# Kernel optimization log

Hardware: AMD Instinct MI355X
Metric: run time of the kernel (lower is better)

## Reference

```python
import jax, jax.numpy as jnp
import numpy as np

IN_F = 256
OUT_F = 256
ALPHA = 0.2  # LeakyReLU negative slope


def _xavier(key, shape, gain=1.414):
    fan_in, fan_out = shape[0], shape[1]
    limit = gain * np.sqrt(6.0 / (fan_in + fan_out))
    return jax.random.uniform(key, shape, jnp.float32, -limit, limit)


def setup_inputs() -> dict:
    key = jax.random.key(0)
    k1, k2, k3, k4, k5, k6 = jax.random.split(key, 6)
    B, N = 8, 2048
    h = jax.random.normal(k1, (B, N, IN_F), jnp.float32)
    adj = jax.random.randint(k2, (B, N, N), 0, 2, jnp.int32)
    lrgt1 = jax.random.normal(k3, (B, N, OUT_F), jnp.float32)
    W1 = _xavier(k4, (IN_F, IN_F))
    W2 = _xavier(k5, (OUT_F, OUT_F))
    a = _xavier(k6, (2 * IN_F, 1))
    return {"h": h, "adj": adj, "lrgt1": lrgt1, "W1": W1, "W2": W2, "a": a}


def reference(h, adj, lrgt1, W1, W2, a):
    # Wh: [B,N,in], wlrgt: [B,N,out]
    Wh = jnp.matmul(h, W1)
    wlrgt = jnp.matmul(lrgt1, W2)
    # additive attention scores: e[b,i,j] = leaky_relu(Wh_i @ a1 + Wh_j @ a2)
    a1 = a[:IN_F, 0]   # [in]
    a2 = a[IN_F:, 0]   # [in]
    Wh1 = jnp.einsum('bnc,c->bn', Wh, a1)  # [B,N]
    Wh2 = jnp.einsum('bnc,c->bn', Wh, a2)  # [B,N]
    e = jax.nn.leaky_relu(Wh1[:, :, None] + Wh2[:, None, :], ALPHA)  # [B,N,N]
    neg = jnp.float32(-9e15)
    masked = jnp.where(adj > 0, e, neg)
    attention = jax.nn.softmax(masked, axis=2)
    # dropout p=0.0 / eval mode -> identity
    h_prime = jnp.matmul(attention, Wh)      # [B,N,in]
    gt_prime = jnp.matmul(attention, wlrgt)  # [B,N,out]
    return (jax.nn.elu(h_prime), jax.nn.elu(gt_prime))
```

## Files before the change

kernel.cpp:

```cpp
#include <hip/hip_runtime.h>
#include <hip/hip_bf16.h>

#define IN_F 256
#define NN   2048
#define BB   8

typedef unsigned short u16;
typedef unsigned long long u64;
typedef __attribute__((ext_vector_type(8))) short short8x;
typedef __attribute__((ext_vector_type(4))) float float4x;

__device__ __forceinline__ u16 f2b(float f) {
    union { float f; unsigned int u; } x; x.f = f;
    unsigned int r = x.u + 0x7FFFu + ((x.u >> 16) & 1u);
    return (u16)(r >> 16);
}

__global__ __launch_bounds__(256) void adjpack(const int* __restrict__ adj,
                                               u64* __restrict__ mask)
{
    const int wid  = (blockIdx.x * 256 + threadIdx.x) >> 6;
    const int lane = threadIdx.x & 63;
#pragma unroll 4
    for (int it = 0; it < 64; ++it) {
        const long s = (long)it * 8192 + wid;
        const int v = __builtin_nontemporal_load(adj + s * 64 + lane);
        const u64 m = __ballot(v > 0);
        if (lane == 0) mask[s] = m;
    }
}

__device__ __forceinline__ void transp_body4(const float* __restrict__ src,
                                             u16* __restrict__ dst,
                                             int R, int C, int tid,
                                             float (*tile)[33])
{
    const int per = (R / 32) * (C / 32);
    const int b  = tid / per;
    const int tt = tid % per;
    const int jt = tt / (C / 32);
    const int ct = tt % (C / 32);
    src += (long)b * R * C;
    dst += (long)b * R * C;

    const int t = threadIdx.x;
    const int lr = t >> 3, lc = (t & 7) * 4;
    float4 v = *(const float4*)(src + (long)(jt * 32 + lr) * C + ct * 32 + lc);
    tile[lr][lc + 0] = v.x;
    tile[lr][lc + 1] = v.y;
    tile[lr][lc + 2] = v.z;
    tile[lr][lc + 3] = v.w;
    __syncthreads();
    const int c = t >> 3, r4 = (t & 7) * 4;
    ushort4 o;
    o.x = f2b(tile[r4 + 0][c]);
    o.y = f2b(tile[r4 + 1][c]);
    o.z = f2b(tile[r4 + 2][c]);
    o.w = f2b(tile[r4 + 3][c]);
    *(ushort4*)(dst + (long)(ct * 32 + c) * R + jt * 32 + r4) = o;
}

__global__ __launch_bounds__(256) void prep(const float* __restrict__ h,
                                            const float* __restrict__ g,
                                            const float* __restrict__ W1,
                                            const float* __restrict__ W2,
                                            const float* __restrict__ a,
                                            u16* __restrict__ HbfT,
                                            u16* __restrict__ GbfT,
                                            u16* __restrict__ W1T,
                                            u16* __restrict__ W2T,
                                            float* __restrict__ v1,
                                            float* __restrict__ v2)
{
    __shared__ float tile[32][33];
    __shared__ float s1[IN_F], s2[IN_F];
    const int bid = blockIdx.x;

    if (bid < 4096) {
        transp_body4(h, HbfT, NN, IN_F, bid, tile);
    } else if (bid < 8192) {
        transp_body4(g, GbfT, NN, IN_F, bid - 4096, tile);
    } else if (bid < 8256) {
        transp_body4(W1, W1T, IN_F, IN_F, bid - 8192, tile);
    } else if (bid < 8320) {
        transp_body4(W2, W2T, IN_F, IN_F, bid - 8256, tile);
    } else {
        const int t = threadIdx.x;
        s1[t] = a[t];
        s2[t] = a[IN_F + t];
        __syncthreads();
        float acc1 = 0.f, acc2 = 0.f;
        for (int c = 0; c < IN_F; ++c) {
            float w = W1[t * IN_F + c];
            acc1 += w * s1[c];
            acc2 += w * s2[c];
        }
        v1[t] = acc1;
        v2[t] = acc2;
    }
}

__global__ __launch_bounds__(256) void rowdots(const float* __restrict__ h,
                                               const float* __restrict__ v1,
                                               const float* __restrict__ v2,
                                               float* __restrict__ Wh1,
                                               float* __restrict__ Wh2)
{
    const int wave = threadIdx.x >> 6;
    const int lane = threadIdx.x & 63;
    const long row = (long)blockIdx.x * 4 + wave;
    const int c0 = lane * 4;

    float4 v  = *(const float4*)(h + row * IN_F + c0);
    float4 a1 = *(const float4*)(v1 + c0);
    float4 a2 = *(const float4*)(v2 + c0);

    float s1 = v.x * a1.x + v.y * a1.y + v.z * a1.z + v.w * a1.w;
    float s2 = v.x * a2.x + v.y * a2.y + v.z * a2.z + v.w * a2.w;
#pragma unroll
    for (int off = 32; off; off >>= 1) {
        s1 += __shfl_xor(s1, off, 64);
        s2 += __shfl_xor(s2, off, 64);
    }
    if (lane == 0) { Wh1[row] = s1; Wh2[row] = s2; }
}

#define KSTEP(ksv, BC, BN_, AC, AN_, do_a, jnxt)                              \
    {                                                                         \
        if (do_a) {                                                           \
            _Pragma("unroll") for (int rt = 0; rt < 4; ++rt)                  \
                AN_[rt] = *(const short8x*)&ab[(((ksv) + 1) * 4 + rt) * 512 + lane * 8]; \
        }                                                                     \
        _Pragma("unroll") for (int ct = 0; ct < 4; ++ct)                      \
            BN_[ct] = *(const short8x*)(Bp + ct * 16 * NN + (jnxt));          \
        _Pragma("unroll") for (int rt = 0; rt < 4; ++rt)                      \
            _Pragma("unroll") for (int ct = 0; ct < 4; ++ct)                  \
                acc[rt][ct] = __builtin_amdgcn_mfma_f32_16x16x32_bf16(AC[rt], BC[ct], acc[rt][ct], 0, 0, 0); \
    }

#define CHUNK9(KCH, MKC, MKN)                                                 \
    {                                                                         \
        const int j0 = (KCH) * 128;                                           \
        const unsigned bits = (MKC) >> ((sg & 1) * 16);                       \
        union { short8x v; u16 e[8]; } pk0, pk1;                              \
        _Pragma("unroll") for (int u = 0; u < 4; ++u) {                       \
            const float4 wv = *(const float4*)&wh2L[j0 + sg * 16 + u * 4];    \
            const float wf[4] = {wv.x, wv.y, wv.z, wv.w};                     \
            _Pragma("unroll") for (int c = 0; c < 4; ++c) {                   \
                float x = wh1rr + wf[c];                                      \
                float ev = fmaxf(x, 0.2f * x);                                \
                float p = __expf(ev - mv);                                    \
                p = ((bits >> (u * 4 + c)) & 1u) ? p : 0.0f;                  \
                lloc += p;                                                    \
                u16 fv = f2b(p);                                              \
                if (u < 2) pk0.e[u * 4 + c] = fv;                             \
                else       pk1.e[(u - 2) * 4 + c] = fv;                       \
            }                                                                 \
        }                                                                     \
        if ((KCH) < 15) MKN = maskR[((KCH) + 1) * 4 + (sg >> 1)];             \
        u16* ab = &Afrag[(KCH) & 1][0];                                       \
        *(short8x*)&ab[wbase0]       = pk0.v;                                 \
        *(short8x*)&ab[wbase0 + 128] = pk1.v;                                 \
        asm volatile("s_waitcnt lgkmcnt(0)\n\ts_barrier" ::: "memory");       \
        _Pragma("unroll") for (int rt = 0; rt < 4; ++rt)                      \
            A0[rt] = *(const short8x*)&ab[rt * 512 + lane * 8];               \
        KSTEP(0, B0, B1, A0, A1, 1, j0 + 1 * 32 + bq8)                        \
        KSTEP(1, B1, B0, A1, A0, 1, j0 + 2 * 32 + bq8)                        \
        KSTEP(2, B0, B1, A0, A1, 1, j0 + 3 * 32 + bq8)                        \
        KSTEP(3, B1, B0, A1, A0, 0, (((KCH) < 15) ? (j0 + 128) : j0) + bq8)   \
    }

__global__ __launch_bounds__(512, 2) void attn_mfma(
    const unsigned* __restrict__ mask,
    const u16* __restrict__ HbfT, const u16* __restrict__ GbfT,
    const float* __restrict__ Wh1, const float* __restrict__ Wh2,
    u16* __restrict__ PH, u16* __restrict__ PG)
{
    const int t = threadIdx.x;
    const int wave = t >> 6, lane = t & 63;
    const int bswz = ((blockIdx.x & 7) << 5) | (blockIdx.x >> 3);
    const int b = bswz >> 5;
    const long gi0 = (long)bswz * 64;

    __shared__ __align__(16) u16 Afrag[2][8192];
    __shared__ float wh2L[2048];
    __shared__ float sred[512];
    __shared__ float ssc[65];

    const int rr = t >> 3, sg = t & 7;
    const float* wh2b = Wh2 + (long)b * NN;
    const float wh1rr = Wh1[gi0 + rr];
    const unsigned* maskR = mask + (gi0 + rr) * 64;

    {
        float4 w = *(const float4*)(wh2b + t * 4);
        *(float4*)&wh2L[t * 4] = w;
        sred[t] = fmaxf(fmaxf(w.x, w.y), fmaxf(w.z, w.w));
    }
    __syncthreads();
    if (t < 64) {
        float v = sred[t * 8];
#pragma unroll
        for (int k = 1; k < 8; ++k) v = fmaxf(v, sred[t * 8 + k]);
#pragma unroll
        for (int off = 32; off; off >>= 1) v = fmaxf(v, __shfl_xor(v, off, 64));
        if (t == 0) ssc[64] = v;
    }
    __syncthreads();
    const float mm = wh1rr + ssc[64];
    const float mv = (mm >= 0.f) ? mm : 0.2f * mm;

    const int wbase0 = ((sg >> 1) * 4 + (rr >> 4)) * 512
                     + ((rr & 15) + 16 * (2 * (sg & 1))) * 8;

    float4x acc[4][4];
#pragma unroll
    for (int rt = 0; rt < 4; ++rt)
#pragma unroll
        for (int ct = 0; ct < 4; ++ct) acc[rt][ct] = (float4x)0.0f;

    const int bn = lane & 15, bq = lane >> 4, bq8 = bq * 8;
    const long hbase = (long)b * IN_F * NN;
    const u16* Bp = ((wave < 4) ? HbfT : GbfT) + hbase
                  + (long)((wave & 3) * 64 + bn) * NN;

    float lloc = 0.f;

    short8x A0[4], A1[4], B0[4], B1[4];
    unsigned mkA, mkB;

    mkA = maskR[sg >> 1];
    mkB = maskR[4 + (sg >> 1)];
#pragma unroll
    for (int ct = 0; ct < 4; ++ct)
        B0[ct] = *(const short8x*)(Bp + ct * 16 * NN + bq8);

    for (int kp = 0; kp < 8; ++kp) {
        CHUNK9(kp * 2,     mkA, mkB)
        CHUNK9(kp * 2 + 1, mkB, mkA)
    }

    sred[t] = lloc;
    __syncthreads();
    if (t < 64) {
        float v = sred[t * 8];
#pragma unroll
        for (int k = 1; k < 8; ++k) v += sred[t * 8 + k];
        ssc[t] = 1.0f / v;
    }
    __syncthreads();

    u16* dst = (wave < 4) ? PH : PG;
    const int colb = (wave & 3) * 64;
#pragma unroll
    for (int rt = 0; rt < 4; ++rt)
#pragma unroll
        for (int ct = 0; ct < 4; ++ct) {
            const int c = colb + ct * 16 + bn;
#pragma unroll
            for (int reg = 0; reg < 4; ++reg) {
                const int rl = rt * 16 + bq * 4 + reg;
                const float il = ssc[rl];
                const long row = gi0 + rl;
                dst[row * IN_F + c] = f2b(acc[rt][ct][reg] * il);
            }
        }
}

__global__ __launch_bounds__(256) void epi2(const u16* __restrict__ PH,
                                            const u16* __restrict__ PG,
                                            const u16* __restrict__ W1T,
                                            const u16* __restrict__ W2T,
                                            float* __restrict__ out)
{
    int bid = blockIdx.x;
    const u16* X;
    const u16* WT;
    float* o;
    if (bid < 512) { X = PH; WT = W1T; o = out; }
    else           { X = PG; WT = W2T; o = out + (long)BB * NN * IN_F; bid -= 512; }

    const int t = threadIdx.x;
    const int wave = t >> 6, lane = t & 63;
    const long i0 = (long)bid * 32;

    __shared__ __align__(16) u16 Afrag[8 * 2 * 64 * 8];

    const int m = t >> 3, ks0 = t & 7, rt0 = m >> 4, lm = m & 15;
    const u16* xp = X + (i0 + m) * IN_F + ks0 * 32;
#pragma unroll
    for (int q = 0; q < 4; ++q) {
        short8x v = *(const short8x*)(xp + q * 8);
        *(short8x*)&Afrag[((ks0 * 2 + rt0) * 64 + lm + q * 16) * 8] = v;
    }
    __syncthreads();

    float4x acc[2][4];
#pragma unroll
    for (int rt = 0; rt < 2; ++rt)
#pragma unroll
        for (int ct = 0; ct < 4; ++ct) acc[rt][ct] = (float4x)0.0f;

    const int bn = lane & 15, bq = lane >> 4;
#pragma unroll
    for (int ks = 0; ks < 8; ++ks) {
        short8x A0 = *(const short8x*)&Afrag[((ks * 2 + 0) * 64 + lane) * 8];
        short8x A1 = *(const short8x*)&Afrag[((ks * 2 + 1) * 64 + lane) * 8];
#pragma unroll
        for (int ct = 0; ct < 4; ++ct) {
            const int n = wave * 64 + ct * 16 + bn;
            short8x Bw = *(const short8x*)(WT + n * IN_F + ks * 32 + bq * 8);
            acc[0][ct] = __builtin_amdgcn_mfma_f32_16x16x32_bf16(A0, Bw, acc[0][ct], 0, 0, 0);
            acc[1][ct] = __builtin_amdgcn_mfma_f32_16x16x32_bf16(A1, Bw, acc[1][ct], 0, 0, 0);
        }
    }

#pragma unroll
    for (int rt = 0; rt < 2; ++rt)
#pragma unroll
        for (int ct = 0; ct < 4; ++ct) {
            const int n = wave * 64 + ct * 16 + bn;
#pragma unroll
            for (int reg = 0; reg < 4; ++reg) {
                const long row = i0 + rt * 16 + bq * 4 + reg;
                float v = acc[rt][ct][reg];
                v = (v > 0.f) ? v : (__expf(v) - 1.f);
                o[row * IN_F + n] = v;
            }
        }
}

extern "C" void kernel_launch(void* const* d_in, const int* in_sizes, int n_in,
                              void* d_out, int out_size, void* d_ws, size_t ws_size,
                              hipStream_t stream)
{
    int ih = -1, ig = -1, iadj = -1, iw1 = -1, iw2 = -1, ia = -1;
    for (int i = 0; i < n_in; ++i) {
        int s = in_sizes[i];
        if      (s == BB * NN * NN)   { if (iadj < 0) iadj = i; }
        else if (s == BB * NN * IN_F) { if (ih < 0) ih = i; else if (ig < 0) ig = i; }
        else if (s == IN_F * IN_F)    { if (iw1 < 0) iw1 = i; else if (iw2 < 0) iw2 = i; }
        else if (s == 2 * IN_F)       { if (ia < 0) ia = i; }
    }
    if (ih < 0 || ig < 0 || iadj < 0 || iw1 < 0 || iw2 < 0 || ia < 0) {
        ih = 0; iadj = 1; ig = 2; iw1 = 3; iw2 = 4; ia = 5;
    }
    const float* h     = (const float*)d_in[ih];
    const int*   adj   = (const int*)  d_in[iadj];
    const float* lrgt1 = (const float*)d_in[ig];
    const float* W1    = (const float*)d_in[iw1];
    const float* W2    = (const float*)d_in[iw2];
    const float* a     = (const float*)d_in[ia];
    float* out = (float*)d_out;

    u64*      mask64 = (u64*)d_out;
    unsigned* mask32 = (unsigned*)d_out;

    float* ws   = (float*)d_ws;
    float* v1   = ws;
    float* v2   = v1 + IN_F;
    float* Wh1  = v2 + IN_F;
    float* Wh2  = Wh1 + BB * NN;
    u16* W1T  = (u16*)(Wh2 + BB * NN);
    u16* W2T  = W1T + IN_F * IN_F;
    u16* HbfT = W2T + IN_F * IN_F;
    u16* GbfT = HbfT + (long)BB * IN_F * NN;
    u16* PH   = GbfT + (long)BB * IN_F * NN;
    u16* PG   = PH + (long)BB * NN * IN_F;

    const int nrows = BB * NN;

    adjpack  <<<2048,        256, 0, stream>>>(adj, mask64);
    prep     <<<8321,        256, 0, stream>>>(h, lrgt1, W1, W2, a,
                                               HbfT, GbfT, W1T, W2T, v1, v2);
    rowdots  <<<nrows / 4,   256, 0, stream>>>(h, v1, v2, Wh1, Wh2);
    attn_mfma<<<nrows / 64,  512, 0, stream>>>(mask32, HbfT, GbfT, Wh1, Wh2, PH, PG);
    epi2     <<<2 * nrows / 32, 256, 0, stream>>>(PH, PG, W1T, W2T, out);
}
```

Before: 344.3 us.

## Prefetch a whole chunk of B fragments ahead in attention and epilogue GEMMs

In the attention kernel, all four B-fragment groups for the next 128-column chunk are loaded into four register sets right after each MFMA group uses them. This gives the global loads a full chunk of softmax and MFMA work to complete under, instead of one k-step. The epilogue GEMM now double-buffers its W fragments, prefetching the next k-step while the current MFMAs run, and issues the first load before the barrier. The extra register sets raise VGPR pressure under launch_bounds(512,2), which could cause spilling or fewer resident waves.

```diff
diff --git a/kernel.cpp b/kernel.cpp
--- a/kernel.cpp
+++ b/kernel.cpp
@@ -125,20 +125,20 @@
     if (lane == 0) { Wh1[row] = s1; Wh2[row] = s2; }
 }
 
-#define KSTEP(ksv, BC, BN_, AC, AN_, do_a, jnxt)                              \
-    {                                                                         \
-        if (do_a) {                                                           \
-            _Pragma("unroll") for (int rt = 0; rt < 4; ++rt)                  \
-                AN_[rt] = *(const short8x*)&ab[(((ksv) + 1) * 4 + rt) * 512 + lane * 8]; \
-        }                                                                     \
+#define AREAD(AR, KS)                                                         \
+    _Pragma("unroll") for (int rt = 0; rt < 4; ++rt)                          \
+        AR[rt] = *(const short8x*)&ab[((KS) * 4 + rt) * 512 + lane * 8];
+
+#define MFMA16(AR, G)                                                         \
+    _Pragma("unroll") for (int rt = 0; rt < 4; ++rt)                          \
         _Pragma("unroll") for (int ct = 0; ct < 4; ++ct)                      \
-            BN_[ct] = *(const short8x*)(Bp + ct * 16 * NN + (jnxt));          \
-        _Pragma("unroll") for (int rt = 0; rt < 4; ++rt)                      \
-            _Pragma("unroll") for (int ct = 0; ct < 4; ++ct)                  \
-                acc[rt][ct] = __builtin_amdgcn_mfma_f32_16x16x32_bf16(AC[rt], BC[ct], acc[rt][ct], 0, 0, 0); \
-    }
-
-#define CHUNK9(KCH, MKC, MKN)                                                 \
+            acc[rt][ct] = __builtin_amdgcn_mfma_f32_16x16x32_bf16(AR[rt], G[ct], acc[rt][ct], 0, 0, 0);
+
+#define BISSUE(G, KN, KS)                                                     \
+    _Pragma("unroll") for (int ct = 0; ct < 4; ++ct)                          \
+        G[ct] = *(const short8x*)(Bp + ct * 16 * NN + ((KN) * 128 + (KS) * 32 + bq8));
+
+#define CHUNK10(KCH, MKC, MKN)                                                \
     {                                                                         \
         const int j0 = (KCH) * 128;                                           \
         const unsigned bits = (MKC) >> ((sg & 1) * 16);                       \
@@ -162,12 +162,18 @@
         *(short8x*)&ab[wbase0]       = pk0.v;                                 \
         *(short8x*)&ab[wbase0 + 128] = pk1.v;                                 \
         asm volatile("s_waitcnt lgkmcnt(0)\n\ts_barrier" ::: "memory");       \
-        _Pragma("unroll") for (int rt = 0; rt < 4; ++rt)                      \
-            A0[rt] = *(const short8x*)&ab[rt * 512 + lane * 8];               \
-        KSTEP(0, B0, B1, A0, A1, 1, j0 + 1 * 32 + bq8)                        \
-        KSTEP(1, B1, B0, A1, A0, 1, j0 + 2 * 32 + bq8)                        \
-        KSTEP(2, B0, B1, A0, A1, 1, j0 + 3 * 32 + bq8)                        \
-        KSTEP(3, B1, B0, A1, A0, 0, (((KCH) < 15) ? (j0 + 128) : j0) + bq8)   \
+        AREAD(Aa, 0)                                                          \
+        AREAD(Ab, 1)                                                          \
+        MFMA16(Aa, G0)                                                        \
+        if ((KCH) < 15) { BISSUE(G0, (KCH) + 1, 0) }                          \
+        AREAD(Aa, 2)                                                          \
+        MFMA16(Ab, G1)                                                        \
+        if ((KCH) < 15) { BISSUE(G1, (KCH) + 1, 1) }                          \
+        AREAD(Ab, 3)                                                          \
+        MFMA16(Aa, G2)                                                        \
+        if ((KCH) < 15) { BISSUE(G2, (KCH) + 1, 2) }                          \
+        MFMA16(Ab, G3)                                                        \
+        if ((KCH) < 15) { BISSUE(G3, (KCH) + 1, 3) }                          \
     }
 
 __global__ __launch_bounds__(512, 2) void attn_mfma(
@@ -226,18 +232,20 @@
 
     float lloc = 0.f;
 
-    short8x A0[4], A1[4], B0[4], B1[4];
+    short8x Aa[4], Ab[4];
+    short8x G0[4], G1[4], G2[4], G3[4];
     unsigned mkA, mkB;
 
     mkA = maskR[sg >> 1];
     mkB = maskR[4 + (sg >> 1)];
-#pragma unroll
-    for (int ct = 0; ct < 4; ++ct)
-        B0[ct] = *(const short8x*)(Bp + ct * 16 * NN + bq8);
+    BISSUE(G0, 0, 0)
+    BISSUE(G1, 0, 1)
+    BISSUE(G2, 0, 2)
+    BISSUE(G3, 0, 3)
 
     for (int kp = 0; kp < 8; ++kp) {
-        CHUNK9(kp * 2,     mkA, mkB)
-        CHUNK9(kp * 2 + 1, mkB, mkA)
+        CHUNK10(kp * 2,     mkA, mkB)
+        CHUNK10(kp * 2 + 1, mkB, mkA)
     }
 
     sred[t] = lloc;
@@ -267,6 +275,20 @@
         }
 }
 
+#define EPIK(KS, BC, BN_)                                                     \
+    {                                                                         \
+        if ((KS) < 7) {                                                       \
+            _Pragma("unroll") for (int ct = 0; ct < 4; ++ct)                  \
+                BN_[ct] = *(const short8x*)(WTrow + ct * 16 * IN_F + ((KS) + 1) * 32 + bq8); \
+        }                                                                     \
+        short8x A0 = *(const short8x*)&Afrag[(((KS) * 2 + 0) * 64 + lane) * 8]; \
+        short8x A1 = *(const short8x*)&Afrag[(((KS) * 2 + 1) * 64 + lane) * 8]; \
+        _Pragma("unroll") for (int ct = 0; ct < 4; ++ct) {                    \
+            acc[0][ct] = __builtin_amdgcn_mfma_f32_16x16x32_bf16(A0, BC[ct], acc[0][ct], 0, 0, 0); \
+            acc[1][ct] = __builtin_amdgcn_mfma_f32_16x16x32_bf16(A1, BC[ct], acc[1][ct], 0, 0, 0); \
+        }                                                                     \
+    }
+
 __global__ __launch_bounds__(256) void epi2(const u16* __restrict__ PH,
                                             const u16* __restrict__ PG,
                                             const u16* __restrict__ W1T,
@@ -293,7 +315,9 @@
         short8x v = *(const short8x*)(xp + q * 8);
         *(short8x*)&Afrag[((ks0 * 2 + rt0) * 64 + lm + q * 16) * 8] = v;
     }
-    __syncthreads();
+
+    const int bn = lane & 15, bq = lane >> 4, bq8 = bq * 8;
+    const u16* WTrow = WT + (long)(wave * 64 + bn) * IN_F;
 
     float4x acc[2][4];
 #pragma unroll
@@ -301,18 +325,17 @@
 #pragma unroll
         for (int ct = 0; ct < 4; ++ct) acc[rt][ct] = (float4x)0.0f;
 
-    const int bn = lane & 15, bq = lane >> 4;
-#pragma unroll
-    for (int ks = 0; ks < 8; ++ks) {
-        short8x A0 = *(const short8x*)&Afrag[((ks * 2 + 0) * 64 + lane) * 8];
-        short8x A1 = *(const short8x*)&Afrag[((ks * 2 + 1) * 64 + lane) * 8];
-#pragma unroll
-        for (int ct = 0; ct < 4; ++ct) {
-            const int n = wave * 64 + ct * 16 + bn;
-            short8x Bw = *(const short8x*)(WT + n * IN_F + ks * 32 + bq * 8);
-            acc[0][ct] = __builtin_amdgcn_mfma_f32_16x16x32_bf16(A0, Bw, acc[0][ct], 0, 0, 0);
-            acc[1][ct] = __builtin_amdgcn_mfma_f32_16x16x32_bf16(A1, Bw, acc[1][ct], 0, 0, 0);
-        }
+    short8x BwA[4], BwB[4];
+#pragma unroll
+    for (int ct = 0; ct < 4; ++ct)
+        BwA[ct] = *(const short8x*)(WTrow + ct * 16 * IN_F + bq8);
+
+    __syncthreads();
+
+#pragma unroll
+    for (int kp2 = 0; kp2 < 4; ++kp2) {
+        EPIK(kp2 * 2,     BwA, BwB)
+        EPIK(kp2 * 2 + 1, BwB, BwA)
     }
 
 #pragma unroll
```

Measured after the change: 335.9 us. -2.4%, faster.
